# Optimization experiments

Hardware: AMD Instinct MI355X
Metric: run time of the kernel (lower is better)

## Reference

```python
import jax, jax.numpy as jnp
import numpy as np

B, HIMG, WIMG = 256, 64, 64
U, K, HID, O, A, V = 8, 4, 128, 4, 7, 400
EMB = ((HIMG - 1) // 2 - 2) * ((WIMG - 1) // 2 - 2) * 64  # 53824
CV = EMB // U  # comm value size 6728
DK, DKC = 64, 32  # input / comm attention key sizes


def conv2d(x, w, b):
    y = jax.lax.conv_general_dilated(x, w, (1, 1), 'VALID',
                                     dimension_numbers=('NCHW', 'OIHW', 'NCHW'))
    return y + b[None, :, None, None]


def maxpool2(x):
    return jax.lax.reduce_window(x, -jnp.inf, jax.lax.max,
                                 (1, 1, 2, 2), (1, 1, 2, 2), 'VALID')


def setup_inputs() -> dict:
    key = jax.random.key(0)
    ks = jax.random.split(key, 26)
    n = lambda i, shape, sc: (jax.random.normal(ks[i], shape, jnp.float32) * sc)
    return {
        'x': jax.random.uniform(ks[0], (B, HIMG, WIMG, 3), jnp.float32),
        'hx': n(1, (B, U, HID), 0.1),
        'cx': n(2, (B, U, HID), 0.1),
        'option': jax.random.uniform(ks[3], (B, O), jnp.float32),
        'conv1_w': n(4, (16, 3, 2, 2), 0.2), 'conv1_b': jnp.zeros((16,), jnp.float32),
        'conv2_w': n(5, (32, 16, 2, 2), 0.1), 'conv2_b': jnp.zeros((32,), jnp.float32),
        'conv3_w': n(6, (64, 32, 2, 2), 0.08), 'conv3_b': jnp.zeros((64,), jnp.float32),
        'Wk': n(7, (EMB, DK), 0.01), 'bk': jnp.zeros((DK,), jnp.float32),
        'Wv': n(8, (EMB, V), 0.01), 'bv': jnp.zeros((V,), jnp.float32),
        'Wq': n(9, (O, U, HID, DK), 0.05),
        'Wi': n(10, (U, V, 4 * HID), 0.05),
        'Wh': n(11, (U, HID, 4 * HID), 0.05),
        'b_lstm': jnp.zeros((U, 4 * HID), jnp.float32),
        'Wqc': n(12, (U, HID, DKC), 0.05),
        'Wkc': n(13, (U, HID, DKC), 0.05),
        'Wvc': n(14, (U, HID, CV), 0.05),
        'Wout': n(15, (U, CV, HID), 0.01),
        'pi_w': n(16, (O, HID, A), 0.05),
        'pi_b': n(17, (O, A), 0.05),
    }


def reference(x, hx, cx, option, conv1_w, conv1_b, conv2_w, conv2_b, conv3_w,
              conv3_b, Wk, bk, Wv, bv, Wq, Wi, Wh, b_lstm, Wqc, Wkc, Wvc,
              Wout, pi_w, pi_b):
    # conv trunk: NHWC -> NCHW (as torch transposes), conv/relu/pool stack
    h = jnp.transpose(x, (0, 3, 1, 2))
    h = maxpool2(jax.nn.relu(conv2d(h, conv1_w, conv1_b)))
    h = jax.nn.relu(conv2d(h, conv2_w, conv2_b))
    h = jax.nn.relu(conv2d(h, conv3_w, conv3_b))
    emb = h.reshape(h.shape[0], -1)  # (B, EMB)

    # RIM input attention: real input + null row, per-unit option-conditioned queries
    xin = jnp.stack([emb, jnp.zeros_like(emb)], axis=1)     # (B, 2, EMB)
    k_in = xin @ Wk + bk                                     # (B, 2, DK)
    v_in = xin @ Wv + bv                                     # (B, 2, V)
    Wq_o = jnp.einsum('bo,ouhk->buhk', option, Wq)           # option-selected query weights
    q = jnp.einsum('buh,buhk->buk', hx, Wq_o)                # (B, U, DK)
    scores = jnp.einsum('buk,bnk->bun', q, k_in) / jnp.sqrt(jnp.float32(DK))
    probs = jax.nn.softmax(scores, axis=-1)                  # (B, U, 2)
    attn_in = jnp.einsum('bun,bnv->buv', probs, v_in)        # (B, U, V)

    # top-k active-unit mask (units attending most to the real input)
    real = probs[:, :, 0]
    _, idx = jax.lax.top_k(real, K)
    mask = jnp.zeros((real.shape[0], U), real.dtype)
    mask = mask.at[jnp.arange(real.shape[0])[:, None], idx].set(1.0)

    # per-unit LSTM (grouped weights)
    pre = (jnp.einsum('buv,uvg->bug', attn_in, Wi)
           + jnp.einsum('buh,uhg->bug', hx, Wh) + b_lstm)
    i_g, f_g, g_g, o_g = jnp.split(pre, 4, axis=-1)
    c_new = jax.nn.sigmoid(f_g) * cx + jax.nn.sigmoid(i_g) * jnp.tanh(g_g)
    h_new = jax.nn.sigmoid(o_g) * jnp.tanh(c_new)

    # communication attention among units; inactive queries masked out
    qc = jnp.einsum('buh,uhk->buk', h_new, Wqc)
    kc = jnp.einsum('buh,uhk->buk', h_new, Wkc)
    vc = jnp.einsum('buh,uhv->buv', h_new, Wvc)              # (B, U, CV)
    cs = jnp.einsum('buk,bnk->bun', qc, kc) / jnp.sqrt(jnp.float32(DKC))
    cp = jax.nn.softmax(cs, axis=-1) * mask[:, :, None]
    ctx = jnp.einsum('bun,bnv->buv', cp, vc)                 # (B, U, CV)
    h_comm = h_new + jnp.einsum('buv,uvh->buh', ctx, Wout)

    m = mask[:, :, None]
    hy = m * h_comm + (1.0 - m) * hx
    cy = m * c_new + (1.0 - m) * cx

    logits = jnp.einsum('buh,oha->boa', hy, pi_w) + pi_b     # (B, O, A)
    action_probs = jax.nn.softmax(logits, axis=-1)
    return action_probs, hy, cy
```

## Files before the change

### kernel.cpp

```cpp
#include <hip/hip_runtime.h>
#include <math.h>

namespace {
constexpr int NB  = 256;
constexpr int NU  = 8;
constexpr int NKT = 4;
constexpr int NH  = 128;
constexpr int NO  = 4;
constexpr int NA  = 7;
constexpr int NV  = 400;
constexpr int NE  = 53824;
constexpr int NCV = 6728;
constexpr int NDK = 64;
constexpr int NDKC= 32;

constexpr int H1 = 31, W1 = 31;
constexpr int H2 = 30, W2 = 30;
constexpr int H3 = 29, W3 = 29;
}

typedef __attribute__((ext_vector_type(8))) short bf16x8_t;
typedef __attribute__((ext_vector_type(4))) float f32x4_t;

__device__ __forceinline__ unsigned short f2bf(float f) {
    unsigned int u = __float_as_uint(f);
    u += 0x7FFFu + ((u >> 16) & 1u);
    return (unsigned short)(u >> 16);
}
__device__ __forceinline__ float bf2f(unsigned short h) {
    return __uint_as_float((unsigned int)h << 16);
}

__global__ __launch_bounds__(256)
void k_conv1(const float* __restrict__ x, const float* __restrict__ w,
             const float* __restrict__ bias, float* __restrict__ out)
{
    __shared__ float ws[16*3*2*2];
    __shared__ float bs[16];
    int tid = threadIdx.x;
    if (tid < 192) ws[tid] = w[tid];
    if (tid < 16)  bs[tid] = bias[tid];
    __syncthreads();
    long idx = (long)blockIdx.x*256 + tid;
    if (idx >= (long)NB*16*H1*W1) return;
    int pw = idx % W1; long t = idx / W1;
    int ph = t % H1; t /= H1;
    int oc = t % 16; int b = t / 16;
    float mx = 0.f;
#pragma unroll
    for (int dh = 0; dh < 2; ++dh)
#pragma unroll
    for (int dw = 0; dw < 2; ++dw) {
        int h = 2*ph + dh, ww = 2*pw + dw;
        float s = bs[oc];
#pragma unroll
        for (int kh = 0; kh < 2; ++kh)
#pragma unroll
        for (int kw = 0; kw < 2; ++kw) {
            const float* xp = x + (((long)b*64 + (h+kh))*64 + (ww+kw))*3;
#pragma unroll
            for (int ic = 0; ic < 3; ++ic)
                s += xp[ic] * ws[((oc*3+ic)*2+kh)*2+kw];
        }
        mx = fmaxf(mx, s);
    }
    out[idx] = mx;
}

template<int OC, int IC, int HIN, int WIN, int HOUT, int WOUT>
__global__ __launch_bounds__(256)
void conv2x2_gemm(const float* __restrict__ in, const float* __restrict__ w,
                  const float* __restrict__ bias, float* __restrict__ out)
{
    constexpr int K    = IC*4;
    constexpr int TY   = OC/4;
    constexpr int TX   = 256/TY;
    constexpr int NT   = TX*4;
    constexpr int SPAT = HOUT*WOUT;
    constexpr int NBLK = (SPAT + NT - 1)/NT;
    constexpr int AIT  = OC*16/256;
    constexpr int BIT  = 16*NT/256;

    const int b  = blockIdx.x / NBLK;
    const int n0 = (blockIdx.x % NBLK) * NT;

    __shared__ __align__(16) float As[2][16][OC+4];
    __shared__ __align__(16) float Bs[2][16][NT];

    const int tid = threadIdx.x;
    const int tx = tid % TX, ty = tid / TX;
    float acc[4][4] = {};
    const float* inb = in + (long)b*IC*HIN*WIN;

    const int nIdx = tid & (NT-1);
    int ohw = 0; bool nOk = false;
    {
        int s = n0 + nIdx;
        if (s < SPAT) { ohw = (s / WOUT) * WIN + (s % WOUT); nOk = true; }
    }

    float aR[AIT], bR[BIT];
    auto loadAB = [&](int kk) {
#pragma unroll
        for (int i = 0; i < AIT; ++i) {
            int lin = tid + i*256;
            aR[i] = w[(lin/16)*K + kk + (lin%16)];
        }
#pragma unroll
        for (int i = 0; i < BIT; ++i) {
            int k = (tid + i*256) / NT;
            int gk = kk + k;
            int ic = gk >> 2, tap = gk & 3;
            bR[i] = nOk ? inb[ic*HIN*WIN + ohw + (tap>>1)*WIN + (tap&1)] : 0.f;
        }
    };
    auto storeAB = [&](int buf) {
#pragma unroll
        for (int i = 0; i < AIT; ++i) {
            int lin = tid + i*256;
            As[buf][lin%16][lin/16] = aR[i];
        }
#pragma unroll
        for (int i = 0; i < BIT; ++i) {
            int k = (tid + i*256) / NT;
            Bs[buf][k][nIdx] = bR[i];
        }
    };

    loadAB(0);
    storeAB(0);
    __syncthreads();
    int cur = 0;
    for (int kk = 0; kk < K; kk += 16) {
        const bool more = (kk + 16 < K);
        if (more) loadAB(kk + 16);
#pragma unroll
        for (int k = 0; k < 16; ++k) {
            float4 a4 = *reinterpret_cast<const float4*>(&As[cur][k][ty*4]);
            float4 b4 = *reinterpret_cast<const float4*>(&Bs[cur][k][tx*4]);
            float av[4] = {a4.x,a4.y,a4.z,a4.w};
            float bw[4] = {b4.x,b4.y,b4.z,b4.w};
#pragma unroll
            for (int i = 0; i < 4; ++i)
#pragma unroll
            for (int j = 0; j < 4; ++j) acc[i][j] += av[i]*bw[j];
        }
        if (more) {
            storeAB(cur ^ 1);
            __syncthreads();
            cur ^= 1;
        }
    }
#pragma unroll
    for (int i = 0; i < 4; ++i) {
        int gm = ty*4 + i;
        float bi = bias[gm];
#pragma unroll
        for (int j = 0; j < 4; ++j) {
            int s = n0 + tx*4 + j;
            if (s < SPAT)
                out[((long)b*OC + gm)*SPAT + s] = fmaxf(acc[i][j] + bi, 0.f);
        }
    }
}

__global__ __launch_bounds__(256)
void k_cvt(const float* __restrict__ in, unsigned short* __restrict__ out, long n)
{
    long i = ((long)blockIdx.x*256 + threadIdx.x) * 8;
    if (i >= n) return;
    float4 a = *(const float4*)(in + i);
    float4 b = *(const float4*)(in + i + 4);
    uint4 u;
    u.x = (unsigned)f2bf(a.x) | ((unsigned)f2bf(a.y) << 16);
    u.y = (unsigned)f2bf(a.z) | ((unsigned)f2bf(a.w) << 16);
    u.z = (unsigned)f2bf(b.x) | ((unsigned)f2bf(b.y) << 16);
    u.w = (unsigned)f2bf(b.z) | ((unsigned)f2bf(b.w) << 16);
    *(uint4*)(out + i) = u;
}

__global__ __launch_bounds__(256)
void k_f2bt(const float* __restrict__ in, unsigned short* __restrict__ out,
            int R, int Cc, long sIn)
{
    __shared__ unsigned short t[32][33];
    const int b = blockIdx.z;
    const int r0 = blockIdx.y * 32, c0 = blockIdx.x * 32;
    const float* ip = in + (long)b * sIn;
    unsigned short* op = out + (long)b * sIn;
    const int tid = threadIdx.x;
    {
        int rr = tid >> 3, c4 = (tid & 7) * 4;
        int gr = r0 + rr;
        unsigned short h0=0,h1=0,h2=0,h3=0;
        if (gr < R) {
            if (c0 + c4 + 3 < Cc) {
                float4 f = *(const float4*)(ip + (long)gr*Cc + c0 + c4);
                h0=f2bf(f.x); h1=f2bf(f.y); h2=f2bf(f.z); h3=f2bf(f.w);
            } else {
                if (c0+c4+0 < Cc) h0 = f2bf(ip[(long)gr*Cc + c0+c4+0]);
                if (c0+c4+1 < Cc) h1 = f2bf(ip[(long)gr*Cc + c0+c4+1]);
                if (c0+c4+2 < Cc) h2 = f2bf(ip[(long)gr*Cc + c0+c4+2]);
                if (c0+c4+3 < Cc) h3 = f2bf(ip[(long)gr*Cc + c0+c4+3]);
            }
        }
        t[rr][c4+0]=h0; t[rr][c4+1]=h1; t[rr][c4+2]=h2; t[rr][c4+3]=h3;
    }
    __syncthreads();
    {
        int cc = tid >> 3, r4 = (tid & 7) * 4;
        int gc = c0 + cc;
        if (gc < Cc && r0 + r4 < R) {
            if (r0 + r4 + 3 < R) {
                *(ushort4*)(op + (long)gc*R + r0 + r4) =
                    make_ushort4(t[r4+0][cc], t[r4+1][cc], t[r4+2][cc], t[r4+3][cc]);
            } else {
#pragma unroll
                for (int j = 0; j < 4; ++j)
                    if (r0 + r4 + j < R) op[(long)gc*R + r0 + r4 + j] = t[r4+j][cc];
            }
        }
    }
}

template<int ROWS, bool F32>
__device__ __forceinline__ void stage_tile(const void* __restrict__ Av, long lda,
                                           int m0, int kk, int kEnd, int Mlim,
                                           unsigned short* lds, int tid)
{
#pragma unroll
    for (int i = 0; i < ROWS/64; ++i) {
        int row = (tid >> 2) + i*64;
        int blk = tid & 3;
        long gm = m0 + row;
        long gk = kk + blk*8;
        ushort4 lo = make_ushort4(0,0,0,0), hi = make_ushort4(0,0,0,0);
        if (gm < Mlim && gk < kEnd) {
            if (F32) {
                const float* A = (const float*)Av + gm*lda + gk;
                float4 f0 = *(const float4*)(A);
                float4 f1 = *(const float4*)(A + 4);
                lo = make_ushort4(f2bf(f0.x),f2bf(f0.y),f2bf(f0.z),f2bf(f0.w));
                hi = make_ushort4(f2bf(f1.x),f2bf(f1.y),f2bf(f1.z),f2bf(f1.w));
            } else {
                const unsigned short* A = (const unsigned short*)Av + gm*lda + gk;
                lo = *(const ushort4*)(A);
                hi = *(const ushort4*)(A + 4);
            }
        }
        int p = (blk ^ (row & 3)) << 3;
        *(ushort4*)&lds[row*32 + p]     = lo;
        *(ushort4*)&lds[row*32 + p + 4] = hi;
    }
}

template<int BM, int BN, bool AF32>
__global__ __launch_bounds__(256)
void bgemm_splitk(const void* __restrict__ Av, long lda, long sA,
                  const unsigned short* __restrict__ BT, long ldbt, long sB,
                  float* __restrict__ Cpart,
                  int M, int N, int K, int nsplit, int kChunk)
{
    constexpr int MR = BM/32, NR = BN/32;
    const int z = blockIdx.z;
    const int batch = z / nsplit, split = z - batch*nsplit;
    const int kStart = split * kChunk;
    const int kEnd = (kStart + kChunk < K) ? (kStart + kChunk) : K;
    const int m0 = blockIdx.y * BM;
    const int n0 = blockIdx.x * BN;

    __shared__ __align__(16) unsigned short As[BM*32];
    __shared__ __align__(16) unsigned short Bs[BN*32];

    const int tid = threadIdx.x;
    const int wave = tid >> 6, lane = tid & 63;
    const int wr = wave >> 1, wc = wave & 1;
    const int lr = lane & 15, lk = lane >> 4;
    const int rbase = wr*(BM/2), cbase = wc*(BN/2);

    const void* Ab = AF32 ? (const void*)((const float*)Av + (long)batch*sA)
                          : (const void*)((const unsigned short*)Av + (long)batch*sA);
    const unsigned short* Bb = BT + (long)batch*sB;

    f32x4_t acc[MR][NR];
#pragma unroll
    for (int i = 0; i < MR; ++i)
#pragma unroll
    for (int j = 0; j < NR; ++j)
        acc[i][j] = (f32x4_t){0.f,0.f,0.f,0.f};

    for (int kk = kStart; kk < kEnd; kk += 32) {
        stage_tile<BM,AF32>(Ab, lda, m0, kk, kEnd, M, As, tid);
        stage_tile<BN,false>((const void*)Bb, ldbt, n0, kk, kEnd, N, Bs, tid);
        __syncthreads();
        bf16x8_t af[MR], bfv[NR];
#pragma unroll
        for (int i = 0; i < MR; ++i) {
            int row = rbase + i*16 + lr;
            af[i] = *(const bf16x8_t*)&As[row*32 + ((lk ^ (row & 3)) << 3)];
        }
#pragma unroll
        for (int j = 0; j < NR; ++j) {
            int col = cbase + j*16 + lr;
            bfv[j] = *(const bf16x8_t*)&Bs[col*32 + ((lk ^ (col & 3)) << 3)];
        }
#pragma unroll
        for (int i = 0; i < MR; ++i)
#pragma unroll
        for (int j = 0; j < NR; ++j)
            acc[i][j] = __builtin_amdgcn_mfma_f32_16x16x32_bf16(af[i], bfv[j], acc[i][j], 0, 0, 0);
        __syncthreads();
    }

    const long cb2 = (long)z * M * N;
#pragma unroll
    for (int i = 0; i < MR; ++i) {
#pragma unroll
        for (int r = 0; r < 4; ++r) {
            int gm = m0 + rbase + i*16 + lk*4 + r;
            if (gm >= M) continue;
#pragma unroll
            for (int j = 0; j < NR; ++j) {
                int gn = n0 + cbase + j*16 + lr;
                if (gn < N) Cpart[cb2 + (long)gm*N + gn] = acc[i][j][r];
            }
        }
    }
}

template<bool AF32>
__global__ __launch_bounds__(256)
void bgemm_direct(const void* __restrict__ Av, long lda, long sA,
                  const unsigned short* __restrict__ BT, long ldbt, long sB,
                  unsigned short* __restrict__ Cout, long ldc, long sC,
                  int M, int N, int K)
{
    const int batch = blockIdx.z;
    const int m0 = blockIdx.y * 128;
    const int n0 = blockIdx.x * 128;

    __shared__ __align__(16) unsigned short As[128*32];
    __shared__ __align__(16) unsigned short Bs[128*32];

    const int tid = threadIdx.x;
    const int wave = tid >> 6, lane = tid & 63;
    const int wr = wave >> 1, wc = wave & 1;
    const int lr = lane & 15, lk = lane >> 4;

    const void* Ab = AF32 ? (const void*)((const float*)Av + (long)batch*sA)
                          : (const void*)((const unsigned short*)Av + (long)batch*sA);
    const unsigned short* Bb = BT + (long)batch*sB;

    f32x4_t acc[4][4];
#pragma unroll
    for (int i = 0; i < 4; ++i)
#pragma unroll
    for (int j = 0; j < 4; ++j)
        acc[i][j] = (f32x4_t){0.f,0.f,0.f,0.f};

    for (int kk = 0; kk < K; kk += 32) {
        stage_tile<128,AF32>(Ab, lda, m0, kk, K, M, As, tid);
        stage_tile<128,false>((const void*)Bb, ldbt, n0, kk, K, N, Bs, tid);
        __syncthreads();
        bf16x8_t af[4], bfv[4];
#pragma unroll
        for (int i = 0; i < 4; ++i) {
            int row = wr*64 + i*16 + lr;
            af[i]  = *(const bf16x8_t*)&As[row*32 + ((lk ^ (row & 3)) << 3)];
            int col = wc*64 + i*16 + lr;
            bfv[i] = *(const bf16x8_t*)&Bs[col*32 + ((lk ^ (col & 3)) << 3)];
        }
#pragma unroll
        for (int i = 0; i < 4; ++i)
#pragma unroll
        for (int j = 0; j < 4; ++j)
            acc[i][j] = __builtin_amdgcn_mfma_f32_16x16x32_bf16(af[i], bfv[j], acc[i][j], 0, 0, 0);
        __syncthreads();
    }

    unsigned short* C = Cout + (long)batch * sC;
#pragma unroll
    for (int i = 0; i < 4; ++i) {
#pragma unroll
        for (int r = 0; r < 4; ++r) {
            int gm = m0 + wr*64 + i*16 + lk*4 + r;
            if (gm >= M) continue;
#pragma unroll
            for (int j = 0; j < 4; ++j) {
                int gn = n0 + wc*64 + j*16 + lr;
                if (gn < N) C[(long)gm*ldc + gn] = f2bf(acc[i][j][r]);
            }
        }
    }
}

template<bool AF32>
__global__ __launch_bounds__(256)
void bgemm_f32(const void* __restrict__ Av, long lda, long sA,
               const unsigned short* __restrict__ BT, long ldbt, long sB,
               float* __restrict__ Cout, long ldc, long sC,
               int M, int N, int K)
{
    const int batch = blockIdx.z;
    const int m0 = blockIdx.y * 64;
    const int n0 = blockIdx.x * 64;

    __shared__ __align__(16) unsigned short As[64*32];
    __shared__ __align__(16) unsigned short Bs[64*32];

    const int tid = threadIdx.x;
    const int wave = tid >> 6, lane = tid & 63;
    const int wr = wave >> 1, wc = wave & 1;
    const int lr = lane & 15, lk = lane >> 4;
    const int rbase = wr*32, cbase = wc*32;

    const void* Ab = AF32 ? (const void*)((const float*)Av + (long)batch*sA)
                          : (const void*)((const unsigned short*)Av + (long)batch*sA);
    const unsigned short* Bb = BT + (long)batch*sB;

    f32x4_t acc[2][2];
#pragma unroll
    for (int i = 0; i < 2; ++i)
#pragma unroll
    for (int j = 0; j < 2; ++j)
        acc[i][j] = (f32x4_t){0.f,0.f,0.f,0.f};

    for (int kk = 0; kk < K; kk += 32) {
        stage_tile<64,AF32>(Ab, lda, m0, kk, K, M, As, tid);
        stage_tile<64,false>((const void*)Bb, ldbt, n0, kk, K, N, Bs, tid);
        __syncthreads();
        bf16x8_t af[2], bfv[2];
#pragma unroll
        for (int i = 0; i < 2; ++i) {
            int row = rbase + i*16 + lr;
            af[i] = *(const bf16x8_t*)&As[row*32 + ((lk ^ (row & 3)) << 3)];
            int col = cbase + i*16 + lr;
            bfv[i] = *(const bf16x8_t*)&Bs[col*32 + ((lk ^ (col & 3)) << 3)];
        }
#pragma unroll
        for (int i = 0; i < 2; ++i)
#pragma unroll
        for (int j = 0; j < 2; ++j)
            acc[i][j] = __builtin_amdgcn_mfma_f32_16x16x32_bf16(af[i], bfv[j], acc[i][j], 0, 0, 0);
        __syncthreads();
    }

    float* C = Cout + (long)batch * sC;
#pragma unroll
    for (int i = 0; i < 2; ++i) {
#pragma unroll
        for (int r = 0; r < 4; ++r) {
            int gm = m0 + rbase + i*16 + lk*4 + r;
            if (gm >= M) continue;
#pragma unroll
            for (int j = 0; j < 2; ++j) {
                int gn = n0 + cbase + j*16 + lr;
                if (gn < N) C[(long)gm*ldc + gn] = acc[i][j][r];
            }
        }
    }
}

__global__ __launch_bounds__(256)
void k0_gemm(const float* __restrict__ A, const float* __restrict__ B,
             float* __restrict__ Cpart, int K, int kChunk)
{
    const int z = blockIdx.x;
    const int kStart = z * kChunk;
    const int kEnd = (kStart + kChunk < K) ? (kStart + kChunk) : K;
    __shared__ __align__(16) float As[16][260];
    __shared__ __align__(16) float Bs[16][64];
    const int tid = threadIdx.x;
    const int tx = tid & 15, ty = tid >> 4;
    float acc[16][4] = {};
    for (int kk = kStart; kk < kEnd; kk += 16) {
#pragma unroll
        for (int i = 0; i < 4; ++i) {
            int row = (tid >> 2) + i*64;
            int k4 = (tid & 3) * 4;
            long gk = kk + k4;
            float4 f = {0,0,0,0};
            if (gk + 3 < (long)kEnd) f = *(const float4*)(A + (long)row*K + gk);
            else {
                if (gk+0 < kEnd) f.x = A[(long)row*K+gk+0];
                if (gk+1 < kEnd) f.y = A[(long)row*K+gk+1];
                if (gk+2 < kEnd) f.z = A[(long)row*K+gk+2];
                if (gk+3 < kEnd) f.w = A[(long)row*K+gk+3];
            }
            As[k4+0][row]=f.x; As[k4+1][row]=f.y; As[k4+2][row]=f.z; As[k4+3][row]=f.w;
        }
        {
            int k = tid >> 4, n = (tid & 15) * 4;
            long gk = kk + k;
            float4 f = {0,0,0,0};
            if (gk < kEnd) f = *(const float4*)(B + gk*64 + n);
            *(float4*)&Bs[k][n] = f;
        }
        __syncthreads();
#pragma unroll
        for (int k = 0; k < 16; ++k) {
            float4 b4 = *reinterpret_cast<const float4*>(&Bs[k][tx*4]);
            float bw[4] = {b4.x,b4.y,b4.z,b4.w};
#pragma unroll
            for (int i4 = 0; i4 < 4; ++i4) {
                float4 a4 = *reinterpret_cast<const float4*>(&As[k][ty*16 + i4*4]);
                float av[4] = {a4.x,a4.y,a4.z,a4.w};
#pragma unroll
                for (int r = 0; r < 4; ++r)
#pragma unroll
                for (int j = 0; j < 4; ++j) acc[i4*4+r][j] += av[r]*bw[j];
            }
        }
        __syncthreads();
    }
    float* cp = Cpart + (long)z*256*64;
#pragma unroll
    for (int i = 0; i < 16; ++i) {
        int gm = ty*16 + i;
#pragma unroll
        for (int j = 0; j < 4; ++j)
            cp[(long)gm*64 + tx*4 + j] = acc[i][j];
    }
}

__global__ __launch_bounds__(256)
void k_reduce_splitk(const float* __restrict__ Cpart, float* __restrict__ out,
                     long ldcOut, long sOut,
                     const float* __restrict__ bias, long sBias,
                     int nbatch, int M, int N, int nsplit)
{
    long idx = (long)blockIdx.x*256 + threadIdx.x;
    long total = (long)nbatch*M*N;
    if (idx >= total) return;
    int n = idx % N; long t = idx / N;
    int m = t % M; int bi = t / M;
    const float* p = Cpart + ((long)bi*nsplit)*((long)M*N) + (long)m*N + n;
    float s = bias ? bias[(long)bi*sBias + n] : 0.f;
#pragma unroll 8
    for (int si = 0; si < nsplit; ++si) s += p[(long)si*M*N];
    out[(long)bi*sOut + (long)m*ldcOut + n] = s;
}

__global__ __launch_bounds__(256)
void k_q(const float* __restrict__ opt, const float* __restrict__ hx,
         const float* __restrict__ Wq, float* __restrict__ q)
{
    int idx = blockIdx.x*256 + threadIdx.x;
    if (idx >= NB*NU*NDK) return;
    int k = idx & 63; int t = idx >> 6;
    int u = t & 7; int b = t >> 3;
    const float* hxr = hx + (long)(b*NU+u)*NH;
    float acc = 0.f;
    for (int o = 0; o < NO; ++o) {
        const float* w = Wq + ((long)(o*NU+u)*NH)*NDK + k;
        float s = 0.f;
        for (int h = 0; h < NH; ++h) s += hxr[h] * w[(long)h*NDK];
        acc += opt[b*NO+o] * s;
    }
    q[idx] = acc;
}

__global__ __launch_bounds__(64)
void k_attn(const float* __restrict__ q, const float* __restrict__ k0,
            const float* __restrict__ bk, const float* __restrict__ v0,
            const float* __restrict__ bv, float* __restrict__ attn,
            float* __restrict__ real)
{
    int bu = blockIdx.x;
    int lane = threadIdx.x;
    int b = bu >> 3;
    float qv = q[(long)bu*NDK + lane];
    float s0 = qv * k0[(long)b*NDK + lane];
    float s1 = qv * bk[lane];
    for (int off = 32; off; off >>= 1) {
        s0 += __shfl_xor(s0, off);
        s1 += __shfl_xor(s1, off);
    }
    s0 *= 0.125f; s1 *= 0.125f;
    float mx = fmaxf(s0, s1);
    float e0 = expf(s0-mx), e1 = expf(s1-mx);
    float inv = 1.f/(e0+e1);
    float p0 = e0*inv, p1 = e1*inv;
    if (lane == 0) real[bu] = p0;
    for (int v = lane; v < NV; v += 64)
        attn[(long)bu*NV + v] = p0*v0[(long)b*NV + v] + p1*bv[v];
}

__global__ void k_topk(const float* __restrict__ real, float* __restrict__ mask)
{
    int b = blockIdx.x*blockDim.x + threadIdx.x;
    if (b >= NB) return;
    float v[NU]; bool sel[NU];
#pragma unroll
    for (int i = 0; i < NU; ++i) { v[i] = real[b*NU+i]; sel[i] = false; }
    for (int t = 0; t < NKT; ++t) {
        int best = 0; float bvv = -1e30f;
#pragma unroll
        for (int i = 0; i < NU; ++i)
            if (!sel[i] && v[i] > bvv) { bvv = v[i]; best = i; }
        sel[best] = true;
    }
#pragma unroll
    for (int i = 0; i < NU; ++i) mask[b*NU+i] = sel[i] ? 1.f : 0.f;
}

__global__ __launch_bounds__(256)
void k_gates(const float* __restrict__ pre_i, const float* __restrict__ pre_h,
             const float* __restrict__ blstm, const float* __restrict__ cx,
             float* __restrict__ cn, float* __restrict__ hn)
{
    int idx = blockIdx.x*256 + threadIdx.x;
    if (idx >= NB*NU*NH) return;
    int h = idx & 127; int bu = idx >> 7;
    int u = bu & 7;
    const float* pi = pre_i + (long)bu*512;
    const float* ph = pre_h + (long)bu*512;
    const float* bl = blstm + (long)u*512;
    float ig = pi[h]     + ph[h]     + bl[h];
    float fg = pi[128+h] + ph[128+h] + bl[128+h];
    float gg = pi[256+h] + ph[256+h] + bl[256+h];
    float og = pi[384+h] + ph[384+h] + bl[384+h];
    float si = 1.f/(1.f+expf(-ig));
    float sf = 1.f/(1.f+expf(-fg));
    float so = 1.f/(1.f+expf(-og));
    float c = sf*cx[idx] + si*tanhf(gg);
    cn[idx] = c;
    hn[idx] = so*tanhf(c);
}

__global__ __launch_bounds__(256)
void k_qckc(const float* __restrict__ hn, const float* __restrict__ Wqc,
            const float* __restrict__ Wkc, float* __restrict__ qc,
            float* __restrict__ kc)
{
    int idx = blockIdx.x*256 + threadIdx.x;
    if (idx >= NB*NU*64) return;
    int j = idx & 63; int t = idx >> 6;
    int u = t & 7; int b = t >> 3;
    int k = j & 31;
    const float* W = (j < 32 ? Wqc : Wkc) + ((long)u*NH)*NDKC + k;
    const float* h = hn + (long)(b*NU+u)*NH;
    float s = 0.f;
    for (int hh = 0; hh < NH; ++hh) s += h[hh]*W[(long)hh*NDKC];
    (j < 32 ? qc : kc)[(b*NU+u)*NDKC + k] = s;
}

__global__ __launch_bounds__(64)
void k_cp(const float* __restrict__ qc, const float* __restrict__ kc,
          const float* __restrict__ mask, float* __restrict__ cp)
{
    int b = blockIdx.x;
    int lane = threadIdx.x;
    int u = lane >> 3, n = lane & 7;
    const float* qr = qc + (long)(b*NU+u)*NDKC;
    const float* kr = kc + (long)(b*NU+n)*NDKC;
    float d = 0.f;
    for (int k = 0; k < NDKC; ++k) d += qr[k]*kr[k];
    d *= 0.17677669529663687f;
    float mx = d;
    for (int off = 4; off; off >>= 1) mx = fmaxf(mx, __shfl_xor(mx, off, 8));
    float e = expf(d-mx);
    float sm = e;
    for (int off = 4; off; off >>= 1) sm += __shfl_xor(sm, off, 8);
    cp[b*64 + lane] = (e/sm) * mask[b*NU+u];
}

__global__ __launch_bounds__(256)
void k_ctx(const unsigned short* __restrict__ vc, const float* __restrict__ cp,
           unsigned short* __restrict__ ctx)
{
    int b = blockIdx.y;
    int v = blockIdx.x*256 + threadIdx.x;
    __shared__ float cps[64];
    if (threadIdx.x < 64) cps[threadIdx.x] = cp[b*64 + threadIdx.x];
    __syncthreads();
    if (v >= NCV) return;
    float vv[NU];
#pragma unroll
    for (int n = 0; n < NU; ++n) vv[n] = bf2f(vc[((long)(b*NU+n))*NCV + v]);
#pragma unroll
    for (int u = 0; u < NU; ++u) {
        float s = 0.f;
#pragma unroll
        for (int n = 0; n < NU; ++n) s += cps[u*8+n]*vv[n];
        ctx[((long)(b*NU+u))*NCV + v] = f2bf(s);
    }
}

__global__ __launch_bounds__(128)
void k_tail(const float* __restrict__ hn, const float* __restrict__ cn,
            const float* __restrict__ hcw, const float* __restrict__ hx,
            const float* __restrict__ cx, const float* __restrict__ mask,
            const float* __restrict__ piw, const float* __restrict__ pib,
            float* __restrict__ hy, float* __restrict__ cy,
            float* __restrict__ out)
{
    const int b = blockIdx.x;
    const int h = threadIdx.x;
    __shared__ float hs[128];
    __shared__ float lg[28];
    float s = 0.f;
#pragma unroll
    for (int u = 0; u < NU; ++u) {
        int idx = (b*NU+u)*NH + h;
        float m = mask[b*NU+u];
        float hyv = m*(hn[idx]+hcw[idx]) + (1.f-m)*hx[idx];
        float cyv = m*cn[idx] + (1.f-m)*cx[idx];
        hy[idx] = hyv; cy[idx] = cyv;
        s += hyv;
    }
    hs[h] = s;
    __syncthreads();
    if (h < 28) {
        int o = h / 7, a = h - o*7;
        float acc = pib[o*NA+a];
        for (int k = 0; k < NH; ++k) acc += hs[k] * piw[((long)o*NH+k)*NA + a];
        lg[h] = acc;
    }
    __syncthreads();
    if (h < NO) {
        float mx = lg[h*NA];
#pragma unroll
        for (int a = 1; a < NA; ++a) mx = fmaxf(mx, lg[h*NA+a]);
        float e[NA]; float sm = 0.f;
#pragma unroll
        for (int a = 0; a < NA; ++a) { e[a] = expf(lg[h*NA+a]-mx); sm += e[a]; }
        float inv = 1.f/sm;
#pragma unroll
        for (int a = 0; a < NA; ++a) out[(long)b*NO*NA + h*NA + a] = e[a]*inv;
    }
}

extern "C" void kernel_launch(void* const* d_in, const int* in_sizes, int n_in,
                              void* d_out, int out_size, void* d_ws, size_t ws_size,
                              hipStream_t stream) {
    const float* x    = (const float*)d_in[0];
    const float* hx   = (const float*)d_in[1];
    const float* cx   = (const float*)d_in[2];
    const float* opt  = (const float*)d_in[3];
    const float* c1w  = (const float*)d_in[4];
    const float* c1b  = (const float*)d_in[5];
    const float* c2w  = (const float*)d_in[6];
    const float* c2b  = (const float*)d_in[7];
    const float* c3w  = (const float*)d_in[8];
    const float* c3b  = (const float*)d_in[9];
    const float* Wk   = (const float*)d_in[10];
    const float* bk   = (const float*)d_in[11];
    const float* Wv   = (const float*)d_in[12];
    const float* bv   = (const float*)d_in[13];
    const float* Wq   = (const float*)d_in[14];
    const float* Wi   = (const float*)d_in[15];
    const float* Wh   = (const float*)d_in[16];
    const float* blstm= (const float*)d_in[17];
    const float* Wqc  = (const float*)d_in[18];
    const float* Wkc  = (const float*)d_in[19];
    const float* Wvc  = (const float*)d_in[20];
    const float* Wout = (const float*)d_in[21];
    const float* piw  = (const float*)d_in[22];
    const float* pib  = (const float*)d_in[23];

    float* out = (float*)d_out;
    float* hy  = out + (long)NB*NO*NA;
    float* cy  = hy + (long)NB*NU*NH;

    float* ws = (float*)d_ws;
    long o = 0;
    float* b_k0  = ws + o; o += 16384;
    float* b_v0  = ws + o; o += 102400;
    float* b_q   = ws + o; o += 131072;
    float* b_at  = ws + o; o += 819200;
    float* b_re  = ws + o; o += 2048;
    float* b_mk  = ws + o; o += 2048;
    float* b_pre = ws + o; o += 1048576;
    float* b_cn  = ws + o; o += 262144;
    float* b_hn  = ws + o; o += 262144;
    float* b_qc  = ws + o; o += 65536;
    float* b_kc  = ws + o; o += 65536;
    float* b_cp  = ws + o; o += 16384;
    float* b_hc  = ws + o; o += 262144;
    float* b_hs  = ws + o; o += 32768;
    constexpr long P1OFF  = 3088384;
    constexpr long C2OFF  = 7024640;
    constexpr long EMBOFF = 14397440;
    constexpr long TOFF   = 28176384;
    constexpr long NEED   = TOFF + 5242880;
    if (ws_size < (size_t)NEED * sizeof(float)) return;

    float* p1    = ws + P1OFF;
    float* c2    = ws + C2OFF;
    float* emb   = ws + EMBOFF;
    float* partK = ws + TOFF;
    float* partV = ws + EMBOFF;
    unsigned short* emb16 = (unsigned short*)(ws + TOFF);
    unsigned short* WvT   = (unsigned short*)(ws + P1OFF);
    unsigned short* WiT   = (unsigned short*)(ws + TOFF);
    unsigned short* WhT   = (unsigned short*)(ws + TOFF + 819200);
    float* pre_h          = ws + TOFF + 819200 + 262144;
    unsigned short* WvcT  = (unsigned short*)(ws + P1OFF);
    unsigned short* WoutT = (unsigned short*)(ws + P1OFF + 3444736);
    float* partW          = ws + P1OFF + 2*3444736;
    unsigned short* vc16  = (unsigned short*)(ws + EMBOFF);
    unsigned short* ctx16 = (unsigned short*)(ws + EMBOFF + 6889472);

    k_conv1<<<(NB*16*H1*W1 + 255)/256, 256, 0, stream>>>(x, c1w, c1b, p1);
    conv2x2_gemm<32,16,H1,W1,H2,W2><<<NB*((H2*W2+127)/128), 256, 0, stream>>>(p1, c2w, c2b, c2);
    conv2x2_gemm<64,32,H2,W2,H3,W3><<<NB*((H3*W3+63)/64), 256, 0, stream>>>(c2, c3w, c3b, emb);

    k_f2bt<<<dim3(13, 1682, 1), 256, 0, stream>>>(Wv, WvT, NE, NV, 0);

    k0_gemm<<<320, 256, 0, stream>>>(emb, Wk, partK, NE, 176);
    k_reduce_splitk<<<(NB*NDK + 255)/256, 256, 0, stream>>>(
        partK, b_k0, NDK, 0, bk, 0, 1, NB, NDK, 320);

    k_cvt<<<((long)NB*NE/8 + 255)/256, 256, 0, stream>>>(emb, emb16, (long)NB*NE);

    bgemm_splitk<128,128,false><<<dim3(4,2,87), 256, 0, stream>>>(
        emb16, NE, 0, WvT, NE, 0, partV, NB, NV, NE, 87, 624);
    k_reduce_splitk<<<(NB*NV + 255)/256, 256, 0, stream>>>(
        partV, b_v0, NV, 0, bv, 0, 1, NB, NV, 87);

    k_q<<<(NB*NU*NDK + 255)/256, 256, 0, stream>>>(opt, hx, Wq, b_q);
    k_attn<<<NB*NU, 64, 0, stream>>>(b_q, b_k0, bk, b_v0, bv, b_at, b_re);
    k_topk<<<1, 256, 0, stream>>>(b_re, b_mk);

    k_f2bt<<<dim3(16, 13, 8), 256, 0, stream>>>(Wi, WiT, NV, 512, (long)NV*512);
    k_f2bt<<<dim3(16, 4, 8), 256, 0, stream>>>(Wh, WhT, NH, 512, (long)NH*512);
    bgemm_f32<true><<<dim3(8, 4, NU), 256, 0, stream>>>(
        b_at, (long)NU*NV, NV, WiT, NV, (long)512*NV,
        b_pre, (long)NU*512, 512, NB, 512, NV);
    bgemm_f32<true><<<dim3(8, 4, NU), 256, 0, stream>>>(
        hx, (long)NU*NH, NH, WhT, NH, (long)512*NH,
        pre_h, (long)NU*512, 512, NB, 512, NH);
    k_gates<<<(NB*NU*NH + 255)/256, 256, 0, stream>>>(b_pre, pre_h, blstm, cx, b_cn, b_hn);

    k_f2bt<<<dim3(211, 4, 8), 256, 0, stream>>>(Wvc, WvcT, NH, NCV, (long)NH*NCV);
    k_f2bt<<<dim3(4, 211, 8), 256, 0, stream>>>(Wout, WoutT, NCV, NH, (long)NCV*NH);

    bgemm_direct<true><<<dim3((NCV+127)/128, 2, NU), 256, 0, stream>>>(
        b_hn, (long)NU*NH, NH, WvcT, NH, (long)NCV*NH,
        vc16, (long)NU*NCV, NCV, NB, NCV, NH);

    k_qckc<<<(NB*NU*64 + 255)/256, 256, 0, stream>>>(b_hn, Wqc, Wkc, b_qc, b_kc);
    k_cp<<<NB, 64, 0, stream>>>(b_qc, b_kc, b_mk, b_cp);
    k_ctx<<<dim3((NCV+255)/256, NB), 256, 0, stream>>>(vc16, b_cp, ctx16);

    bgemm_splitk<64,64,false><<<dim3(2,4,NU*16), 256, 0, stream>>>(
        ctx16, (long)NU*NCV, NCV, WoutT, NCV, (long)NCV*NH,
        partW, NB, NH, NCV, 16, 448);
    k_reduce_splitk<<<(NU*NB*NH + 255)/256, 256, 0, stream>>>(
        partW, b_hc, (long)NU*NH, NH, nullptr, 0, NU, NB, NH, 16);

    k_tail<<<NB, 128, 0, stream>>>(b_hn, b_cn, b_hc, hx, cx, b_mk, piw, pib, hy, cy, out);
}
```

Before: 459.9 us.

## Run conv3 on MFMA using split-bf16 hi/lo emulation of fp32

Replaces the scalar-FMA implicit-GEMM conv3 with an MFMA kernel that splits fp32 operands into bf16 high and low parts and accumulates three bf16 MFMA products to approximate fp32 precision. Weights and im2col input tiles are staged in swizzled shared memory, with 128 output pixels per block across 4 waves. The aim is to move conv3's FMA-bound compute onto matrix cores. In exchange it adds conversion overhead, uncoalesced gather loads for the im2col tile, and a small precision loss from dropping the lo×lo term.

```diff
diff --git a/kernel.cpp b/kernel.cpp
--- a/kernel.cpp
+++ b/kernel.cpp
@@ -160,6 +160,120 @@
             int s = n0 + tx*4 + j;
             if (s < SPAT)
                 out[((long)b*OC + gm)*SPAT + s] = fmaxf(acc[i][j] + bi, 0.f);
+        }
+    }
+}
+
+__global__ __launch_bounds__(256)
+void conv3_mfma(const float* __restrict__ c2, const float* __restrict__ w,
+                const float* __restrict__ bias, float* __restrict__ emb)
+{
+    constexpr int SPAT = 29*29;
+    constexpr int WIN  = 30;
+    const int b  = blockIdx.y;
+    const int n0 = blockIdx.x * 128;
+
+    __shared__ __align__(16) unsigned short Ah[4*64*32], Al[4*64*32];
+    __shared__ __align__(16) unsigned short Bh[128*32],  Bl[128*32];
+
+    const int tid = threadIdx.x;
+    const int wave = tid >> 6, lane = tid & 63;
+    const int wr = wave >> 1, wc = wave & 1;
+    const int lr = lane & 15, lk = lane >> 4;
+    const int rbase = wr*32, cbase = wc*64;
+
+    const float* c2b = c2 + (long)b*32*900;
+
+    {
+        int row = tid >> 2, kb = tid & 3;
+        int p = (kb ^ (row & 3)) << 3;
+#pragma unroll
+        for (int c = 0; c < 4; ++c) {
+            unsigned short hh[8], ll[8];
+#pragma unroll
+            for (int j = 0; j < 8; ++j) {
+                float v = w[(long)row*128 + c*32 + kb*8 + j];
+                unsigned short h = f2bf(v);
+                hh[j] = h; ll[j] = f2bf(v - bf2f(h));
+            }
+            *(ushort4*)&Ah[c*2048 + row*32 + p]     = make_ushort4(hh[0],hh[1],hh[2],hh[3]);
+            *(ushort4*)&Ah[c*2048 + row*32 + p + 4] = make_ushort4(hh[4],hh[5],hh[6],hh[7]);
+            *(ushort4*)&Al[c*2048 + row*32 + p]     = make_ushort4(ll[0],ll[1],ll[2],ll[3]);
+            *(ushort4*)&Al[c*2048 + row*32 + p + 4] = make_ushort4(ll[4],ll[5],ll[6],ll[7]);
+        }
+    }
+
+    const int br0 = tid >> 2, br1 = br0 + 64;
+    const int kb  = tid & 3;
+    int base0 = 0, base1 = 0; bool ok0, ok1;
+    { int s = n0 + br0; ok0 = s < SPAT; if (ok0) base0 = (s/29)*WIN + (s%29); }
+    { int s = n0 + br1; ok1 = s < SPAT; if (ok1) base1 = (s/29)*WIN + (s%29); }
+
+    f32x4_t acc[2][4];
+#pragma unroll
+    for (int i = 0; i < 2; ++i)
+#pragma unroll
+    for (int j = 0; j < 4; ++j) acc[i][j] = (f32x4_t){0.f,0.f,0.f,0.f};
+
+    for (int c = 0; c < 4; ++c) {
+        __syncthreads();
+#pragma unroll
+        for (int rr = 0; rr < 2; ++rr) {
+            int row   = rr ? br1 : br0;
+            bool ok   = rr ? ok1 : ok0;
+            int base  = rr ? base1 : base0;
+            int p = (kb ^ (row & 3)) << 3;
+            unsigned short hh[8], ll[8];
+#pragma unroll
+            for (int j = 0; j < 8; ++j) {
+                int gk = c*32 + kb*8 + j;
+                int ic = gk >> 2, tap = gk & 3;
+                float v = ok ? c2b[ic*900 + base + (tap>>1)*WIN + (tap&1)] : 0.f;
+                unsigned short h = f2bf(v);
+                hh[j] = h; ll[j] = f2bf(v - bf2f(h));
+            }
+            *(ushort4*)&Bh[row*32 + p]     = make_ushort4(hh[0],hh[1],hh[2],hh[3]);
+            *(ushort4*)&Bh[row*32 + p + 4] = make_ushort4(hh[4],hh[5],hh[6],hh[7]);
+            *(ushort4*)&Bl[row*32 + p]     = make_ushort4(ll[0],ll[1],ll[2],ll[3]);
+            *(ushort4*)&Bl[row*32 + p + 4] = make_ushort4(ll[4],ll[5],ll[6],ll[7]);
+        }
+        __syncthreads();
+        bf16x8_t ah[2], al[2], bh[4], bl[4];
+#pragma unroll
+        for (int i = 0; i < 2; ++i) {
+            int row = rbase + i*16 + lr;
+            int off = c*2048 + row*32 + ((lk ^ (row & 3)) << 3);
+            ah[i] = *(const bf16x8_t*)&Ah[off];
+            al[i] = *(const bf16x8_t*)&Al[off];
+        }
+#pragma unroll
+        for (int j = 0; j < 4; ++j) {
+            int col = cbase + j*16 + lr;
+            int off = col*32 + ((lk ^ (col & 3)) << 3);
+            bh[j] = *(const bf16x8_t*)&Bh[off];
+            bl[j] = *(const bf16x8_t*)&Bl[off];
+        }
+#pragma unroll
+        for (int i = 0; i < 2; ++i)
+#pragma unroll
+        for (int j = 0; j < 4; ++j) {
+            acc[i][j] = __builtin_amdgcn_mfma_f32_16x16x32_bf16(ah[i], bh[j], acc[i][j], 0,0,0);
+            acc[i][j] = __builtin_amdgcn_mfma_f32_16x16x32_bf16(ah[i], bl[j], acc[i][j], 0,0,0);
+            acc[i][j] = __builtin_amdgcn_mfma_f32_16x16x32_bf16(al[i], bh[j], acc[i][j], 0,0,0);
+        }
+    }
+
+#pragma unroll
+    for (int i = 0; i < 2; ++i)
+#pragma unroll
+    for (int r = 0; r < 4; ++r) {
+        int gm = rbase + i*16 + lk*4 + r;
+        float bi = bias[gm];
+#pragma unroll
+        for (int j = 0; j < 4; ++j) {
+            int gn = n0 + cbase + j*16 + lr;
+            if (gn < SPAT)
+                emb[((long)b*64 + gm)*SPAT + gn] = fmaxf(acc[i][j][r] + bi, 0.f);
         }
     }
 }
@@ -804,7 +918,7 @@
 
     k_conv1<<<(NB*16*H1*W1 + 255)/256, 256, 0, stream>>>(x, c1w, c1b, p1);
     conv2x2_gemm<32,16,H1,W1,H2,W2><<<NB*((H2*W2+127)/128), 256, 0, stream>>>(p1, c2w, c2b, c2);
-    conv2x2_gemm<64,32,H2,W2,H3,W3><<<NB*((H3*W3+63)/64), 256, 0, stream>>>(c2, c3w, c3b, emb);
+    conv3_mfma<<<dim3((H3*W3+127)/128, NB), 256, 0, stream>>>(c2, c3w, c3b, emb);
 
     k_f2bt<<<dim3(13, 1682, 1), 256, 0, stream>>>(Wv, WvT, NE, NV, 0);
 
```

After: 443.3 us. -3.6%, faster.
